# Optimization experiments

Hardware: AMD Instinct MI355X
Metric: run time of the kernel (lower is better)

## Reference

```python
import jax, jax.numpy as jnp
import numpy as np

K = 3      # kernel size
PAD = 1    # padding


def setup_inputs() -> dict:
    key = jax.random.key(0)
    k1, k2, k3, k4 = jax.random.split(key, 4)
    B, C, H, W, O = 8, 3, 512, 512, 16
    x = jax.random.normal(k1, (B, C, H, W), dtype=jnp.float32)
    offsets = jax.random.normal(k2, (B, 2 * K * K, H, W), dtype=jnp.float32)
    weight = jax.random.normal(k3, (O, C, K, K), dtype=jnp.float32) * 0.1
    bias = jax.random.normal(k4, (O,), dtype=jnp.float32) * 0.1
    return {"x": x, "offsets": offsets, "weight": weight, "bias": bias}


def _deform_conv2d(x, offsets, weight, bias):
    # x: [B,C,H,W]; offsets: [B,2*K*K,H,W] with (dy,dx) interleaved per tap
    B, C, H, W = x.shape
    KK = K * K
    ky = jnp.arange(KK) // K
    kx = jnp.arange(KK) % K
    # base sampling grid (stride=1, dilation=1): p = out_pos - PAD + tap
    base_y = (ky[:, None, None] - PAD + jnp.arange(H)[None, :, None]).astype(x.dtype)  # [KK,H,1]
    base_x = (kx[:, None, None] - PAD + jnp.arange(W)[None, None, :]).astype(x.dtype)  # [KK,1,W]
    py = offsets[:, 0::2] + base_y[None]  # [B,KK,H,W]
    px = offsets[:, 1::2] + base_x[None]  # [B,KK,H,W]

    def sample(img, py_b, px_b):  # img [C,H,W]; py_b,px_b [KK,H,W]
        y0 = jnp.floor(py_b)
        x0 = jnp.floor(px_b)
        wy = py_b - y0  # fractional parts
        wx = px_b - x0
        y0i = y0.astype(jnp.int32)
        x0i = x0.astype(jnp.int32)

        def gather(yi, xi):
            valid = (yi >= 0) & (yi < H) & (xi >= 0) & (xi < W)
            yc = jnp.clip(yi, 0, H - 1)
            xc = jnp.clip(xi, 0, W - 1)
            return img[:, yc, xc] * valid[None].astype(img.dtype)  # [C,KK,H,W]

        v00 = gather(y0i, x0i)
        v01 = gather(y0i, x0i + 1)
        v10 = gather(y0i + 1, x0i)
        v11 = gather(y0i + 1, x0i + 1)
        return (v00 * ((1 - wy) * (1 - wx))[None]
                + v01 * ((1 - wy) * wx)[None]
                + v10 * (wy * (1 - wx))[None]
                + v11 * (wy * wx)[None])

    sampled = jax.vmap(sample)(x, py, px)  # [B,C,KK,H,W]
    O = weight.shape[0]
    out = jnp.einsum('bckhw,ock->bohw', sampled, weight.reshape(O, C, KK))
    return out + bias[None, :, None, None]


def reference(x, offsets, weight, bias):
    return _deform_conv2d(x, offsets, weight, bias)
```

## Files before the change

### kernel.cpp

```cpp
#include <hip/hip_runtime.h>


#define Bc 8
#define Cc 3
#define Hc 512
#define Wc 512
#define Oc 16
#define HWc (512 * 512)
#define KKc 9

__global__ __launch_bounds__(256) void dcn_kernel(
    const float* __restrict__ x,
    const float* __restrict__ offsets,
    const float* __restrict__ weight,
    const float* __restrict__ bias,
    float* __restrict__ out) {
  int pix = blockIdx.x * 256 + threadIdx.x;
  int b = pix >> 18;
  int hw = pix & (HWc - 1);
  int h = hw >> 9;
  int w = hw & 511;

  const float* xb = x + b * (Cc * HWc);
  const float* ob = offsets + b * (2 * KKc * HWc) + hw;

  float acc[Oc];
#pragma unroll
  for (int o = 0; o < Oc; ++o) acc[o] = bias[o];

  const float fh = (float)(h - 1);
  const float fw = (float)(w - 1);

#pragma unroll
  for (int kk = 0; kk < KKc; ++kk) {
    const int ky = kk / 3;
    const int kx = kk % 3;
    float oy = ob[(2 * kk) * HWc];
    float ox = ob[(2 * kk + 1) * HWc];
    float py = oy + fh + (float)ky;
    float px = ox + fw + (float)kx;
    float y0f = floorf(py);
    float x0f = floorf(px);
    float wy = py - y0f;
    float wx = px - x0f;
    int y0 = (int)y0f;
    int x0 = (int)x0f;
    int y1 = y0 + 1;
    int x1 = x0 + 1;

    float vy0 = ((unsigned)y0 < (unsigned)Hc) ? 1.f : 0.f;
    float vy1 = ((unsigned)y1 < (unsigned)Hc) ? 1.f : 0.f;
    float vx0 = ((unsigned)x0 < (unsigned)Wc) ? 1.f : 0.f;
    float vx1 = ((unsigned)x1 < (unsigned)Wc) ? 1.f : 0.f;
    float wy0 = 1.f - wy;
    float wx0 = 1.f - wx;
    float w00 = (wy0 * wx0) * (vy0 * vx0);
    float w01 = (wy0 * wx) * (vy0 * vx1);
    float w10 = (wy * wx0) * (vy1 * vx0);
    float w11 = (wy * wx) * (vy1 * vx1);

    int y0c = min(max(y0, 0), Hc - 1);
    int y1c = min(max(y1, 0), Hc - 1);
    int x0c = min(max(x0, 0), Wc - 1);
    int x1c = min(max(x1, 0), Wc - 1);
    int a00 = (y0c << 9) + x0c;
    int a01 = (y0c << 9) + x1c;
    int a10 = (y1c << 9) + x0c;
    int a11 = (y1c << 9) + x1c;

    float val[Cc];
#pragma unroll
    for (int c = 0; c < Cc; ++c) {
      const float* xc = xb + c * HWc;
      float v00 = xc[a00];
      float v01 = xc[a01];
      float v10 = xc[a10];
      float v11 = xc[a11];
      val[c] = v00 * w00 + v01 * w01 + v10 * w10 + v11 * w11;
    }

    const float* wk = weight + kk;
#pragma unroll
    for (int o = 0; o < Oc; ++o) {
#pragma unroll
      for (int c = 0; c < Cc; ++c) {
        acc[o] = fmaf(wk[o * (Cc * KKc) + c * KKc], val[c], acc[o]);
      }
    }
  }

  float* op = out + b * (Oc * HWc) + hw;
#pragma unroll
  for (int o = 0; o < Oc; ++o) op[o * HWc] = acc[o];
}

extern "C" void kernel_launch(void* const* d_in, const int* in_sizes, int n_in,
                              void* d_out, int out_size, void* d_ws, size_t ws_size,
                              hipStream_t stream) {
  const float* x = (const float*)d_in[0];
  const float* offsets = (const float*)d_in[1];
  const float* weight = (const float*)d_in[2];
  const float* bias = (const float*)d_in[3];
  float* out = (float*)d_out;

  const int total = Bc * HWc;
  dim3 grid(total / 256);
  dim3 block(256);
  hipLaunchKernelGGL(dcn_kernel, grid, block, 0, stream, x, offsets, weight, bias, out);
}
```

Before: 384.0 us.

## Transpose input to packed float4 channel layout for vectorized bilinear gathers

Adds a pre-pass that converts x from CHW planes into a per-pixel float4 (3 channels plus padding) buffer in workspace, so each bilinear corner fetch becomes one 16-byte load instead of three scattered scalar loads. The main kernel also computes all tap addresses and weights up front to expose more memory-level parallelism, and uses nontemporal loads and stores for streaming offsets and outputs. This costs an extra kernel launch and a read and write of the input (about 33% padded), plus higher register pressure. If the workspace is too small, the old kernel runs as a fallback.

```diff
diff --git a/kernel.cpp b/kernel.cpp
--- a/kernel.cpp
+++ b/kernel.cpp
@@ -9,8 +9,22 @@
 #define HWc (512 * 512)
 #define KKc 9
 
-__global__ __launch_bounds__(256) void dcn_kernel(
-    const float* __restrict__ x,
+__global__ __launch_bounds__(256) void transpose_kernel(
+    const float* __restrict__ x, float4* __restrict__ xt) {
+  int pix = blockIdx.x * 256 + threadIdx.x;
+  int b = pix >> 18;
+  int hw = pix & (HWc - 1);
+  const float* xb = x + b * (Cc * HWc) + hw;
+  float4 v;
+  v.x = xb[0];
+  v.y = xb[HWc];
+  v.z = xb[2 * HWc];
+  v.w = 0.f;
+  xt[pix] = v;
+}
+
+__global__ __launch_bounds__(256, 4) void dcn_main(
+    const float4* __restrict__ xt,
     const float* __restrict__ offsets,
     const float* __restrict__ weight,
     const float* __restrict__ bias,
@@ -21,22 +35,20 @@
   int h = hw >> 9;
   int w = hw & 511;
 
-  const float* xb = x + b * (Cc * HWc);
+  const float4* xb = xt + (b << 18);
   const float* ob = offsets + b * (2 * KKc * HWc) + hw;
-
-  float acc[Oc];
-#pragma unroll
-  for (int o = 0; o < Oc; ++o) acc[o] = bias[o];
 
   const float fh = (float)(h - 1);
   const float fw = (float)(w - 1);
 
+  int addr[KKc][4];
+  float wt[KKc][4];
 #pragma unroll
   for (int kk = 0; kk < KKc; ++kk) {
     const int ky = kk / 3;
     const int kx = kk % 3;
-    float oy = ob[(2 * kk) * HWc];
-    float ox = ob[(2 * kk + 1) * HWc];
+    float oy = __builtin_nontemporal_load(&ob[(2 * kk) * HWc]);
+    float ox = __builtin_nontemporal_load(&ob[(2 * kk + 1) * HWc]);
     float py = oy + fh + (float)ky;
     float px = ox + fw + (float)kx;
     float y0f = floorf(py);
@@ -54,41 +66,109 @@
     float vx1 = ((unsigned)x1 < (unsigned)Wc) ? 1.f : 0.f;
     float wy0 = 1.f - wy;
     float wx0 = 1.f - wx;
-    float w00 = (wy0 * wx0) * (vy0 * vx0);
-    float w01 = (wy0 * wx) * (vy0 * vx1);
-    float w10 = (wy * wx0) * (vy1 * vx0);
-    float w11 = (wy * wx) * (vy1 * vx1);
+    wt[kk][0] = (wy0 * wx0) * (vy0 * vx0);
+    wt[kk][1] = (wy0 * wx) * (vy0 * vx1);
+    wt[kk][2] = (wy * wx0) * (vy1 * vx0);
+    wt[kk][3] = (wy * wx) * (vy1 * vx1);
 
     int y0c = min(max(y0, 0), Hc - 1);
     int y1c = min(max(y1, 0), Hc - 1);
     int x0c = min(max(x0, 0), Wc - 1);
     int x1c = min(max(x1, 0), Wc - 1);
-    int a00 = (y0c << 9) + x0c;
-    int a01 = (y0c << 9) + x1c;
-    int a10 = (y1c << 9) + x0c;
-    int a11 = (y1c << 9) + x1c;
+    addr[kk][0] = (y0c << 9) + x0c;
+    addr[kk][1] = (y0c << 9) + x1c;
+    addr[kk][2] = (y1c << 9) + x0c;
+    addr[kk][3] = (y1c << 9) + x1c;
+  }
 
+  float acc[Oc];
+#pragma unroll
+  for (int o = 0; o < Oc; ++o) acc[o] = bias[o];
+
+#pragma unroll
+  for (int kk = 0; kk < KKc; ++kk) {
+    float4 v00 = xb[addr[kk][0]];
+    float4 v01 = xb[addr[kk][1]];
+    float4 v10 = xb[addr[kk][2]];
+    float4 v11 = xb[addr[kk][3]];
+    float w00 = wt[kk][0], w01 = wt[kk][1], w10 = wt[kk][2], w11 = wt[kk][3];
+
+    float val0 = v00.x * w00 + v01.x * w01 + v10.x * w10 + v11.x * w11;
+    float val1 = v00.y * w00 + v01.y * w01 + v10.y * w10 + v11.y * w11;
+    float val2 = v00.z * w00 + v01.z * w01 + v10.z * w10 + v11.z * w11;
+
+    const float* wk = weight + kk;
+#pragma unroll
+    for (int o = 0; o < Oc; ++o) {
+      acc[o] = fmaf(wk[o * 27 + 0], val0,
+               fmaf(wk[o * 27 + 9], val1,
+               fmaf(wk[o * 27 + 18], val2, acc[o])));
+    }
+  }
+
+  float* op = out + b * (Oc * HWc) + hw;
+#pragma unroll
+  for (int o = 0; o < Oc; ++o)
+    __builtin_nontemporal_store(acc[o], &op[o * HWc]);
+}
+
+__global__ __launch_bounds__(256) void dcn_fallback(
+    const float* __restrict__ x,
+    const float* __restrict__ offsets,
+    const float* __restrict__ weight,
+    const float* __restrict__ bias,
+    float* __restrict__ out) {
+  int pix = blockIdx.x * 256 + threadIdx.x;
+  int b = pix >> 18;
+  int hw = pix & (HWc - 1);
+  int h = hw >> 9;
+  int w = hw & 511;
+  const float* xb = x + b * (Cc * HWc);
+  const float* ob = offsets + b * (2 * KKc * HWc) + hw;
+  float acc[Oc];
+#pragma unroll
+  for (int o = 0; o < Oc; ++o) acc[o] = bias[o];
+  const float fh = (float)(h - 1);
+  const float fw = (float)(w - 1);
+#pragma unroll
+  for (int kk = 0; kk < KKc; ++kk) {
+    const int ky = kk / 3;
+    const int kx = kk % 3;
+    float oy = ob[(2 * kk) * HWc];
+    float ox = ob[(2 * kk + 1) * HWc];
+    float py = oy + fh + (float)ky;
+    float px = ox + fw + (float)kx;
+    float y0f = floorf(py), x0f = floorf(px);
+    float wy = py - y0f, wx = px - x0f;
+    int y0 = (int)y0f, x0 = (int)x0f, y1 = y0 + 1, x1 = x0 + 1;
+    float vy0 = ((unsigned)y0 < (unsigned)Hc) ? 1.f : 0.f;
+    float vy1 = ((unsigned)y1 < (unsigned)Hc) ? 1.f : 0.f;
+    float vx0 = ((unsigned)x0 < (unsigned)Wc) ? 1.f : 0.f;
+    float vx1 = ((unsigned)x1 < (unsigned)Wc) ? 1.f : 0.f;
+    float wy0 = 1.f - wy, wx0 = 1.f - wx;
+    float w00 = (wy0 * wx0) * (vy0 * vx0);
+    float w01 = (wy0 * wx) * (vy0 * vx1);
+    float w10 = (wy * wx0) * (vy1 * vx0);
+    float w11 = (wy * wx) * (vy1 * vx1);
+    int y0c = min(max(y0, 0), Hc - 1);
+    int y1c = min(max(y1, 0), Hc - 1);
+    int x0c = min(max(x0, 0), Wc - 1);
+    int x1c = min(max(x1, 0), Wc - 1);
+    int a00 = (y0c << 9) + x0c, a01 = (y0c << 9) + x1c;
+    int a10 = (y1c << 9) + x0c, a11 = (y1c << 9) + x1c;
     float val[Cc];
 #pragma unroll
     for (int c = 0; c < Cc; ++c) {
       const float* xc = xb + c * HWc;
-      float v00 = xc[a00];
-      float v01 = xc[a01];
-      float v10 = xc[a10];
-      float v11 = xc[a11];
-      val[c] = v00 * w00 + v01 * w01 + v10 * w10 + v11 * w11;
+      val[c] = xc[a00] * w00 + xc[a01] * w01 + xc[a10] * w10 + xc[a11] * w11;
     }
-
     const float* wk = weight + kk;
 #pragma unroll
-    for (int o = 0; o < Oc; ++o) {
+    for (int o = 0; o < Oc; ++o)
 #pragma unroll
-      for (int c = 0; c < Cc; ++c) {
-        acc[o] = fmaf(wk[o * (Cc * KKc) + c * KKc], val[c], acc[o]);
-      }
-    }
+      for (int c = 0; c < Cc; ++c)
+        acc[o] = fmaf(wk[o * 27 + c * 9], val[c], acc[o]);
   }
-
   float* op = out + b * (Oc * HWc) + hw;
 #pragma unroll
   for (int o = 0; o < Oc; ++o) op[o * HWc] = acc[o];
@@ -104,7 +184,16 @@
   float* out = (float*)d_out;
 
   const int total = Bc * HWc;
-  dim3 grid(total / 256);
-  dim3 block(256);
-  hipLaunchKernelGGL(dcn_kernel, grid, block, 0, stream, x, offsets, weight, bias, out);
+  const size_t xt_bytes = (size_t)total * 16;
+  dim3 grid(total / 256), block(256);
+
+  if (ws_size >= xt_bytes) {
+    float4* xt = (float4*)d_ws;
+    hipLaunchKernelGGL(transpose_kernel, grid, block, 0, stream, x, xt);
+    hipLaunchKernelGGL(dcn_main, grid, block, 0, stream,
+                       (const float4*)xt, offsets, weight, bias, out);
+  } else {
+    hipLaunchKernelGGL(dcn_fallback, grid, block, 0, stream,
+                       x, offsets, weight, bias, out);
+  }
 }
```

Result: faster. 369.2 us (-3.9%).
